# Kernel optimization log

Measured on AMD Instinct MI355X. Metric: run time of the kernel, lower is better.

## Reference

```python
import jax, jax.numpy as jnp
import numpy as np

EPS = 1e-12  # F.normalize eps

def _l2norm(v):
    n = jnp.sqrt(jnp.sum(v * v, axis=-1, keepdims=True))
    return v / jnp.maximum(n, EPS)

def setup_inputs() -> dict:
    key = jax.random.key(0)
    k1, k2, k3 = jax.random.split(key, 3)
    B, C, H, Wd = 32, 256, 64, 64
    M = 64
    x = jax.random.normal(k1, (B, C, H, Wd), dtype=jnp.float32)
    stdv = 1.0 / np.sqrt(M)
    W = jax.random.uniform(k2, (M, C), dtype=jnp.float32, minval=-stdv, maxval=stdv)
    label_batch = jax.random.randint(k3, (B,), 0, 2)
    return {"x": x, "W": W, "label_batch": label_batch}

def reference(x, W, label_batch):
    B, C, H, Wd = x.shape
    M = W.shape[0]
    # [B, HW, C] tokens; key == query == flattened input (pos=False)
    tok = x.transpose(0, 2, 3, 1).reshape(B, H * Wd, C)
    # per-pixel contribution to each prototype, softmax over pixels (dim=1)
    proto_weight = jax.nn.softmax(jnp.einsum('bnc,mc->bnm', tok, W), axis=1)
    # prototypes [B, M, C], L2-normalized
    proto = _l2norm(jnp.einsum('bnm,bnc->bmc', proto_weight, tok))
    # relevance of each pixel to each prototype, softmax over prototypes
    score = jax.nn.softmax(jnp.einsum('bnc,bmc->bnm', tok, proto), axis=-1)
    # reconstructed query
    new_query = _l2norm(jnp.einsum('bnm,bmc->bnc', score, proto))
    # compact loss: MSE(keys, nearest prototype) (new_cpt == 'True')
    top1 = jnp.argmax(score, axis=-1)                      # [B, HW]
    pos = jnp.take_along_axis(proto, top1[:, :, None], axis=1)  # [B, HW, C]
    compact_loss = jnp.mean((tok - pos) ** 2)
    # distance loss: push prototypes apart
    p2 = jnp.sum(proto * proto, axis=-1)                   # [B, M]
    sqd = p2[:, :, None] + p2[:, None, :] - 2.0 * jnp.einsum('bmc,bkc->bmk', proto, proto)
    dis = 1.0 - sqd
    dis = dis * (dis > 0).astype(dis.dtype)
    dis = jnp.triu(dis, k=1)
    dis_loss = jnp.mean(jnp.sum(dis, axis=(1, 2)) * 2.0 / (M * (M - 1)))
    out = new_query.transpose(0, 2, 1).reshape(B, C, H, Wd)
    return (out, compact_loss, dis_loss)
```

## Files before the change

### kernel.cpp

```cpp
#include <hip/hip_runtime.h>
#include <math.h>

#define B 32
#define C 256
#define M 64
#define N 4096

typedef __attribute__((ext_vector_type(8))) short s16x8;
typedef __attribute__((ext_vector_type(8))) __bf16 bf16x8;
typedef __attribute__((ext_vector_type(4))) float f32x4;
typedef __attribute__((ext_vector_type(4))) unsigned short u16x4;
typedef __attribute__((ext_vector_type(8))) unsigned short u16x8;

static constexpr float EPS = 1e-12f;

__device__ __forceinline__ unsigned short f2bf(float f) {
    unsigned u = __float_as_uint(f);
    u += 0x7FFFu + ((u >> 16) & 1u);
    return (unsigned short)(u >> 16);
}
__device__ __forceinline__ float bf2f(unsigned short h) {
    return __uint_as_float((unsigned)h << 16);
}
__device__ __forceinline__ f32x4 MFMA(s16x8 a, s16x8 b, f32x4 c) {
    return __builtin_amdgcn_mfma_f32_16x16x32_bf16(
        __builtin_bit_cast(bf16x8, a), __builtin_bit_cast(bf16x8, b), c, 0, 0, 0);
}
__device__ __forceinline__ s16x8 cvt8(const f32x4 a, const f32x4 b) {
    bf16x8 h;
    h[0] = (__bf16)a[0]; h[1] = (__bf16)a[1]; h[2] = (__bf16)a[2]; h[3] = (__bf16)a[3];
    h[4] = (__bf16)b[0]; h[5] = (__bf16)b[1]; h[6] = (__bf16)b[2]; h[7] = (__bf16)b[3];
    return __builtin_bit_cast(s16x8, h);
}
__device__ __forceinline__ int swz(int n) {
    return (((n >> 2) & 3) | ((n & 1) << 2)) << 3;
}

__global__ __launch_bounds__(256) void kW_convert(const float* __restrict__ Wf,
                                                  unsigned short* __restrict__ Wb) {
    const int i = blockIdx.x * 256 + threadIdx.x;
    Wb[i] = f2bf(Wf[i]);
}

__global__ __launch_bounds__(256) void k01(const float* __restrict__ x,
                                           const unsigned short* __restrict__ Wb,
                                           unsigned short* __restrict__ xbt,
                                           unsigned short* __restrict__ Sb,
                                           float* __restrict__ xsq) {
    const int nb = blockIdx.x, b = blockIdx.y;
    const int t = threadIdx.x;
    __shared__ unsigned short tsT[64 * 256];
    __shared__ float xred[16][68];
    const int nq = t & 15, cq = t >> 4;
    float part[4] = {0.f, 0.f, 0.f, 0.f};
    const float* xrow = x + (size_t)b * C * N + (size_t)nb * 64 + 4 * nq;
#pragma unroll
    for (int step = 0; step < 4; ++step) {
        const int c0 = cq * 4 + step * 64;
        f32x4 q[4];
#pragma unroll
        for (int i = 0; i < 4; ++i) q[i] = *(const f32x4*)(xrow + (size_t)(c0 + i) * N);
#pragma unroll
        for (int k = 0; k < 4; ++k) {
            const int n = 4 * nq + k;
            u16x4 h;
#pragma unroll
            for (int i = 0; i < 4; ++i) {
                part[k] += q[i][k] * q[i][k];
                h[i] = f2bf(q[i][k]);
            }
            *(u16x4*)(&tsT[n * 256 + (c0 ^ swz(n))]) = h;
        }
    }
#pragma unroll
    for (int k = 0; k < 4; ++k) xred[cq][4 * nq + k] = part[k];
    __syncthreads();
    if (t < 64) {
        float s = 0.f;
#pragma unroll
        for (int j = 0; j < 16; ++j) s += xred[j][t];
        xsq[(size_t)b * N + nb * 64 + t] = s;
    }
    {
        const int l = t & 31, nh = t >> 5;
#pragma unroll
        for (int j = 0; j < 8; ++j) {
            const int n = nh + 8 * j;
            const int c0 = l * 8;
            const u16x8 v = *(const u16x8*)(&tsT[n * 256 + (c0 ^ swz(n))]);
            *(u16x8*)(xbt + ((size_t)b * N + nb * 64 + n) * C + c0) = v;
        }
    }
    const int wv = t >> 6, lane = t & 63, li = lane & 15, lk = lane >> 4;
    const f32x4 zv = {0.f, 0.f, 0.f, 0.f};
    f32x4 acc[4] = {zv, zv, zv, zv};
    const unsigned short* br = Wb + (size_t)(wv * 16 + li) * C + lk * 8;
#pragma unroll
    for (int c0 = 0; c0 < C; c0 += 32) {
        const s16x8 bfrag = *(const s16x8*)(br + c0);
#pragma unroll
        for (int s = 0; s < 4; ++s) {
            const int n = s * 16 + li;
            const s16x8 a = *(const s16x8*)(&tsT[n * 256 + ((lk * 8 + c0) ^ swz(n))]);
            acc[s] = MFMA(a, bfrag, acc[s]);
        }
    }
    unsigned short* Srow = Sb + ((size_t)b * M + wv * 16 + li) * N + nb * 64;
#pragma unroll
    for (int s = 0; s < 4; ++s) {
        u16x4 h;
#pragma unroll
        for (int r = 0; r < 4; ++r) h[r] = f2bf(acc[s][r]);
        *(u16x4*)(Srow + s * 16 + lk * 4) = h;
    }
}

__global__ __launch_bounds__(256) void k2_softmax_n(const unsigned short* __restrict__ Sb,
                                                    unsigned short* __restrict__ Pb) {
    const int m = blockIdx.x, b = blockIdx.y;
    const unsigned short* col = Sb + ((size_t)b * M + m) * N;
    unsigned short* po = Pb + ((size_t)b * M + m) * N;
    const int t = threadIdx.x;
    float v[16];
    const u16x8 h0 = *(const u16x8*)(col + t * 16);
    const u16x8 h1 = *(const u16x8*)(col + t * 16 + 8);
#pragma unroll
    for (int i = 0; i < 8; ++i) v[i] = bf2f(h0[i]);
#pragma unroll
    for (int i = 0; i < 8; ++i) v[8 + i] = bf2f(h1[i]);
    float mx = -INFINITY;
#pragma unroll
    for (int i = 0; i < 16; ++i) mx = fmaxf(mx, v[i]);
#pragma unroll
    for (int off = 32; off >= 1; off >>= 1) mx = fmaxf(mx, __shfl_xor(mx, off));
    __shared__ float redm[4], reds[4];
    const int wave = t >> 6, lane = t & 63;
    if (lane == 0) redm[wave] = mx;
    __syncthreads();
    mx = fmaxf(fmaxf(redm[0], redm[1]), fmaxf(redm[2], redm[3]));
    float s = 0.f;
#pragma unroll
    for (int i = 0; i < 16; ++i) {
        v[i] = __expf(v[i] - mx);
        s += v[i];
    }
#pragma unroll
    for (int off = 32; off >= 1; off >>= 1) s += __shfl_xor(s, off);
    if (lane == 0) reds[wave] = s;
    __syncthreads();
    s = reds[0] + reds[1] + reds[2] + reds[3];
    const float inv = 1.f / s;
    u16x8 o0, o1;
#pragma unroll
    for (int i = 0; i < 8; ++i) o0[i] = f2bf(v[i] * inv);
#pragma unroll
    for (int i = 0; i < 8; ++i) o1[i] = f2bf(v[8 + i] * inv);
    *(u16x8*)(po + t * 16) = o0;
    *(u16x8*)(po + t * 16 + 8) = o1;
}

__global__ __launch_bounds__(256) void k3_mfma(const float* __restrict__ x,
                                               const unsigned short* __restrict__ Pb,
                                               float* __restrict__ parts) {
    const int ck = blockIdx.x, b = blockIdx.y;
    const int wv = threadIdx.x >> 6, lane = threadIdx.x & 63;
    const int li = lane & 15, lk = lane >> 4;
    const int c0w = wv * 64;
    const int nb = ck * 512;
    const f32x4 zv = {0.f, 0.f, 0.f, 0.f};
    f32x4 acc[4][4];
#pragma unroll
    for (int s = 0; s < 4; ++s)
#pragma unroll
        for (int u = 0; u < 4; ++u) acc[s][u] = zv;
    const float* ar = x + ((size_t)b * C + c0w + li) * N + nb + lk * 8;
    const unsigned short* br = Pb + ((size_t)b * M + li) * N + nb + lk * 8;
#pragma unroll 4
    for (int n0 = 0; n0 < 512; n0 += 32) {
        s16x8 af[4], bf_[4];
#pragma unroll
        for (int s = 0; s < 4; ++s) {
            const float* p = ar + (size_t)(s * 16) * N + n0;
            af[s] = cvt8(*(const f32x4*)p, *(const f32x4*)(p + 4));
        }
#pragma unroll
        for (int u = 0; u < 4; ++u) bf_[u] = *(const s16x8*)(br + (size_t)(u * 16) * N + n0);
#pragma unroll
        for (int s = 0; s < 4; ++s)
#pragma unroll
            for (int u = 0; u < 4; ++u) acc[s][u] = MFMA(af[s], bf_[u], acc[s][u]);
    }
    float* pp = parts + ((size_t)b * 8 + ck) * M * C;
#pragma unroll
    for (int s = 0; s < 4; ++s)
#pragma unroll
        for (int u = 0; u < 4; ++u)
            *(f32x4*)(pp + (size_t)(u * 16 + li) * C + c0w + s * 16 + lk * 4) = acc[s][u];
}

__global__ __launch_bounds__(256) void k3b_reduce(const float* __restrict__ parts,
                                                  unsigned short* __restrict__ proto_bf,
                                                  unsigned short* __restrict__ protoT_bf,
                                                  float* __restrict__ p2) {
    const int mb = blockIdx.x, b = blockIdx.y;
    const int t = threadIdx.x;
    const int ml = t >> 5, cl = t & 31;
    const int m = mb * 8 + ml;
    const int c0 = cl * 8;
    float v[8] = {0.f, 0.f, 0.f, 0.f, 0.f, 0.f, 0.f, 0.f};
    const float* pbase = parts + (size_t)b * 8 * M * C + (size_t)m * C + c0;
#pragma unroll
    for (int ck = 0; ck < 8; ++ck) {
        const f32x4 q0 = *(const f32x4*)(pbase + (size_t)ck * M * C);
        const f32x4 q1 = *(const f32x4*)(pbase + (size_t)ck * M * C + 4);
#pragma unroll
        for (int j = 0; j < 4; ++j) { v[j] += q0[j]; v[4 + j] += q1[j]; }
    }
    float sq = 0.f;
#pragma unroll
    for (int j = 0; j < 8; ++j) sq += v[j] * v[j];
#pragma unroll
    for (int off = 16; off >= 1; off >>= 1) sq += __shfl_xor(sq, off);
    const float denom = fmaxf(sqrtf(sq), EPS);
    const float scale = 1.f / denom;
    if (cl == 0) p2[b * M + m] = sq / (denom * denom);
    u16x8 h;
#pragma unroll
    for (int j = 0; j < 8; ++j) h[j] = f2bf(v[j] * scale);
    *(u16x8*)(proto_bf + ((size_t)b * M + m) * C + c0) = h;
#pragma unroll
    for (int j = 0; j < 8; ++j)
        protoT_bf[((size_t)b * C + c0 + j) * M + m] = h[j];
}

__global__ __launch_bounds__(512) void k4f(const unsigned short* __restrict__ proto_bf,
                                           const unsigned short* __restrict__ protoT_bf,
                                           const unsigned short* __restrict__ xbt,
                                           const float* __restrict__ p2,
                                           const float* __restrict__ xsq,
                                           float* __restrict__ out,
                                           float* __restrict__ cparts) {
    const int b = blockIdx.y;
    const int t = threadIdx.x;
    const int w = t >> 6, lane = t & 63, li = lane & 15, lk = lane >> 4;
    const int nblk = blockIdx.x * 256;
    __shared__ unsigned short p_lds[256 * 64];
    __shared__ float red2[2][256];
    __shared__ float red8[8];
    const f32x4 zv = {0.f, 0.f, 0.f, 0.f};
    f32x4 acc[4][2];
#pragma unroll
    for (int s = 0; s < 4; ++s)
#pragma unroll
        for (int u = 0; u < 2; ++u) acc[s][u] = zv;
    const unsigned short* ar = proto_bf + (size_t)b * M * C + (size_t)li * C + lk * 8;
    const unsigned short* br = xbt + ((size_t)b * N + nblk + w * 32 + li) * C + lk * 8;
#pragma unroll
    for (int c0 = 0; c0 < C; c0 += 32) {
        s16x8 af[4], bf_[2];
#pragma unroll
        for (int s = 0; s < 4; ++s) af[s] = *(const s16x8*)(ar + (size_t)(s * 16) * C + c0);
#pragma unroll
        for (int u = 0; u < 2; ++u) bf_[u] = *(const s16x8*)(br + (size_t)(u * 16) * C + c0);
#pragma unroll
        for (int s = 0; s < 4; ++s)
#pragma unroll
            for (int u = 0; u < 2; ++u) acc[s][u] = MFMA(af[s], bf_[u], acc[s][u]);
    }
    float csum = 0.f;
#pragma unroll
    for (int u = 0; u < 2; ++u) {
        const int n = nblk + w * 32 + u * 16 + li;
        const int nl = w * 32 + u * 16 + li;
        float vmax = -INFINITY;
#pragma unroll
        for (int s = 0; s < 4; ++s)
#pragma unroll
            for (int r = 0; r < 4; ++r) vmax = fmaxf(vmax, acc[s][u][r]);
        vmax = fmaxf(vmax, __shfl_xor(vmax, 16));
        vmax = fmaxf(vmax, __shfl_xor(vmax, 32));
        int t1 = 1 << 30;
#pragma unroll
        for (int s = 0; s < 4; ++s)
#pragma unroll
            for (int r = 0; r < 4; ++r)
                if (acc[s][u][r] == vmax) t1 = min(t1, s * 16 + lk * 4 + r);
        t1 = min(t1, __shfl_xor(t1, 16));
        t1 = min(t1, __shfl_xor(t1, 32));
        float es = 0.f;
#pragma unroll
        for (int s = 0; s < 4; ++s)
#pragma unroll
            for (int r = 0; r < 4; ++r) {
                const float e = __expf(acc[s][u][r] - vmax);
                acc[s][u][r] = e;
                es += e;
            }
        es += __shfl_xor(es, 16);
        es += __shfl_xor(es, 32);
        const float inv = 1.f / es;
#pragma unroll
        for (int s = 0; s < 4; ++s) {
            u16x4 h;
#pragma unroll
            for (int r = 0; r < 4; ++r) h[r] = f2bf(acc[s][u][r] * inv);
            const unsigned off =
                (unsigned)((nl * 128 + ((s * 16 + lk * 4) << 1)) ^ ((nl & 7) << 4));
            *(u16x4*)((char*)p_lds + off) = h;
        }
        if (lk == 0) csum += xsq[(size_t)b * N + n] - 2.f * vmax + p2[b * M + t1];
    }
#pragma unroll
    for (int off = 32; off >= 1; off >>= 1) csum += __shfl_xor(csum, off);
    if (lane == 0) red8[w] = csum;
    __syncthreads();
    if (t == 0) {
        float cs = 0.f;
#pragma unroll
        for (int j = 0; j < 8; ++j) cs += red8[j];
        cparts[b * 16 + blockIdx.x] = cs;
    }
    const int nq = w & 3, ch = w >> 2;
    f32x4 a2[4][8];
#pragma unroll
    for (int s = 0; s < 4; ++s)
#pragma unroll
        for (int u = 0; u < 8; ++u) a2[s][u] = zv;
    const unsigned short* br2 =
        protoT_bf + ((size_t)b * C + ch * 128 + li) * M + lk * 8;
#pragma unroll
    for (int m0 = 0; m0 < M; m0 += 32) {
        s16x8 af2[4], bf2[8];
#pragma unroll
        for (int s = 0; s < 4; ++s) {
            const int nl = nq * 64 + s * 16 + li;
            const unsigned off =
                (unsigned)((nl * 128 + ((m0 + lk * 8) << 1)) ^ ((nl & 7) << 4));
            af2[s] = *(const s16x8*)((const char*)p_lds + off);
        }
#pragma unroll
        for (int u = 0; u < 8; ++u)
            bf2[u] = *(const s16x8*)(br2 + (size_t)(u * 16) * M + m0);
#pragma unroll
        for (int s = 0; s < 4; ++s)
#pragma unroll
            for (int u = 0; u < 8; ++u) a2[s][u] = MFMA(af2[s], bf2[u], a2[s][u]);
    }
    float ssq[4][4];
#pragma unroll
    for (int s = 0; s < 4; ++s)
#pragma unroll
        for (int r = 0; r < 4; ++r) {
            float sum = 0.f;
#pragma unroll
            for (int u = 0; u < 8; ++u) sum += a2[s][u][r] * a2[s][u][r];
#pragma unroll
            for (int off = 8; off >= 1; off >>= 1) sum += __shfl_xor(sum, off);
            ssq[s][r] = sum;
        }
    if (li == 0) {
#pragma unroll
        for (int s = 0; s < 4; ++s)
#pragma unroll
            for (int r = 0; r < 4; ++r)
                red2[ch][nq * 64 + s * 16 + lk * 4 + r] = ssq[s][r];
    }
    __syncthreads();
    float scl[4][4];
#pragma unroll
    for (int s = 0; s < 4; ++s)
#pragma unroll
        for (int r = 0; r < 4; ++r) {
            const int nl = nq * 64 + s * 16 + lk * 4 + r;
            scl[s][r] = 1.f / fmaxf(sqrtf(red2[0][nl] + red2[1][nl]), EPS);
        }
    float* ob = out + (size_t)b * C * N;
#pragma unroll
    for (int s = 0; s < 4; ++s)
#pragma unroll
        for (int u = 0; u < 8; ++u) {
            const int c = ch * 128 + u * 16 + li;
            f32x4 q;
#pragma unroll
            for (int r = 0; r < 4; ++r) q[r] = a2[s][u][r] * scl[s][r];
            *(f32x4*)(ob + (size_t)c * N + nblk + nq * 64 + s * 16 + lk * 4) = q;
        }
}

__global__ __launch_bounds__(256) void k4_score(const unsigned short* __restrict__ proto_bf,
                                                const unsigned short* __restrict__ xbt,
                                                const float* __restrict__ p2,
                                                const float* __restrict__ xsq,
                                                unsigned short* __restrict__ pnm,
                                                float* __restrict__ cparts) {
    const int b = blockIdx.y;
    const int wv = threadIdx.x >> 6, lane = threadIdx.x & 63;
    const int li = lane & 15, lk = lane >> 4;
    const int nbase = blockIdx.x * 256 + wv * 64;
    const f32x4 zv = {0.f, 0.f, 0.f, 0.f};
    f32x4 acc[4][4];
#pragma unroll
    for (int s = 0; s < 4; ++s)
#pragma unroll
        for (int u = 0; u < 4; ++u) acc[s][u] = zv;
    const unsigned short* ar = proto_bf + ((size_t)b * M + li) * C + lk * 8;
    const unsigned short* br = xbt + ((size_t)b * N + nbase + li) * C + lk * 8;
#pragma unroll
    for (int c0 = 0; c0 < C; c0 += 32) {
        s16x8 af[4], bf_[4];
#pragma unroll
        for (int s = 0; s < 4; ++s) af[s] = *(const s16x8*)(ar + (size_t)(s * 16) * C + c0);
#pragma unroll
        for (int u = 0; u < 4; ++u) bf_[u] = *(const s16x8*)(br + (size_t)(u * 16) * C + c0);
#pragma unroll
        for (int s = 0; s < 4; ++s)
#pragma unroll
            for (int u = 0; u < 4; ++u) acc[s][u] = MFMA(af[s], bf_[u], acc[s][u]);
    }
    float csum = 0.f;
#pragma unroll
    for (int u = 0; u < 4; ++u) {
        const int n = nbase + u * 16 + li;
        float vmax = -INFINITY;
#pragma unroll
        for (int s = 0; s < 4; ++s)
#pragma unroll
            for (int r = 0; r < 4; ++r) vmax = fmaxf(vmax, acc[s][u][r]);
        vmax = fmaxf(vmax, __shfl_xor(vmax, 16));
        vmax = fmaxf(vmax, __shfl_xor(vmax, 32));
        int t1 = 1 << 30;
#pragma unroll
        for (int s = 0; s < 4; ++s)
#pragma unroll
            for (int r = 0; r < 4; ++r)
                if (acc[s][u][r] == vmax) t1 = min(t1, s * 16 + lk * 4 + r);
        t1 = min(t1, __shfl_xor(t1, 16));
        t1 = min(t1, __shfl_xor(t1, 32));
        float es = 0.f;
#pragma unroll
        for (int s = 0; s < 4; ++s)
#pragma unroll
            for (int r = 0; r < 4; ++r) {
                const float e = __expf(acc[s][u][r] - vmax);
                acc[s][u][r] = e;
                es += e;
            }
        es += __shfl_xor(es, 16);
        es += __shfl_xor(es, 32);
        const float inv = 1.f / es;
        unsigned short* prow = pnm + ((size_t)b * N + n) * M;
#pragma unroll
        for (int s = 0; s < 4; ++s) {
            u16x4 h;
#pragma unroll
            for (int r = 0; r < 4; ++r) h[r] = f2bf(acc[s][u][r] * inv);
            *(u16x4*)(prow + s * 16 + lk * 4) = h;
        }
        if (lk == 0) csum += xsq[(size_t)b * N + n] - 2.f * vmax + p2[b * M + t1];
    }
#pragma unroll
    for (int off = 32; off >= 1; off >>= 1) csum += __shfl_xor(csum, off);
    __shared__ float red[4];
    if (lane == 0) red[wv] = csum;
    __syncthreads();
    if (threadIdx.x == 0)
        cparts[b * 16 + blockIdx.x] = red[0] + red[1] + red[2] + red[3];
}

__global__ __launch_bounds__(256) void k4b_mfma(const unsigned short* __restrict__ pnm,
                                                const unsigned short* __restrict__ protoT_bf,
                                                float* __restrict__ out) {
    const int b = blockIdx.y;
    const int wv = threadIdx.x >> 6, lane = threadIdx.x & 63;
    const int li = lane & 15, lk = lane >> 4;
    const int n0 = blockIdx.x * 64;
    const int cb = wv * 64;
    const f32x4 zv = {0.f, 0.f, 0.f, 0.f};
    f32x4 acc[4][4];
#pragma unroll
    for (int s = 0; s < 4; ++s)
#pragma unroll
        for (int u = 0; u < 4; ++u) acc[s][u] = zv;
    const unsigned short* ar = pnm + ((size_t)b * N + n0 + li) * M + lk * 8;
    const unsigned short* br = protoT_bf + ((size_t)b * C + cb + li) * M + lk * 8;
#pragma unroll
    for (int m0 = 0; m0 < M; m0 += 32) {
        s16x8 af[4], bf_[4];
#pragma unroll
        for (int s = 0; s < 4; ++s) af[s] = *(const s16x8*)(ar + (size_t)(s * 16) * M + m0);
#pragma unroll
        for (int u = 0; u < 4; ++u) bf_[u] = *(const s16x8*)(br + (size_t)(u * 16) * M + m0);
#pragma unroll
        for (int s = 0; s < 4; ++s)
#pragma unroll
            for (int u = 0; u < 4; ++u) acc[s][u] = MFMA(af[s], bf_[u], acc[s][u]);
    }
    __shared__ float ls[4][64];
    __shared__ float ls2[64];
    float psq[4][4];
#pragma unroll
    for (int s = 0; s < 4; ++s)
#pragma unroll
        for (int r = 0; r < 4; ++r) {
            float sum = 0.f;
#pragma unroll
            for (int u = 0; u < 4; ++u) sum += acc[s][u][r] * acc[s][u][r];
#pragma unroll
            for (int off = 8; off >= 1; off >>= 1) sum += __shfl_xor(sum, off);
            psq[s][r] = sum;
        }
    if (li == 0) {
#pragma unroll
        for (int s = 0; s < 4; ++s)
#pragma unroll
            for (int r = 0; r < 4; ++r) ls[wv][s * 16 + lk * 4 + r] = psq[s][r];
    }
    __syncthreads();
    if (threadIdx.x < 64) {
        const int tt = threadIdx.x;
        const float tot = ls[0][tt] + ls[1][tt] + ls[2][tt] + ls[3][tt];
        ls2[tt] = 1.f / fmaxf(sqrtf(tot), EPS);
    }
    __syncthreads();
    float scl[4][4];
#pragma unroll
    for (int s = 0; s < 4; ++s)
#pragma unroll
        for (int r = 0; r < 4; ++r) scl[s][r] = ls2[s * 16 + lk * 4 + r];
    float* ob = out + (size_t)b * C * N;
#pragma unroll
    for (int s = 0; s < 4; ++s)
#pragma unroll
        for (int u = 0; u < 4; ++u) {
            f32x4 q;
#pragma unroll
            for (int r = 0; r < 4; ++r) q[r] = acc[s][u][r] * scl[s][r];
            *(f32x4*)(ob + (size_t)(cb + u * 16 + li) * N + n0 + s * 16 + lk * 4) = q;
        }
}

__global__ __launch_bounds__(256) void k5_dis(const unsigned short* __restrict__ proto_bf,
                                              const float* __restrict__ p2,
                                              float* __restrict__ dparts) {
    const int q = blockIdx.x;
    const int b = blockIdx.y;
    const unsigned short* pr = proto_bf + (size_t)b * M * C;
    __shared__ float pl[M * C];
    for (int idx = threadIdx.x; idx < M * C; idx += 256) {
        int m = idx >> 8, c = idx & 255;
        pl[m * 256 + (c ^ (m & 31))] = bf2f(pr[idx]);
    }
    __syncthreads();
    float sum = 0.f;
    for (int k = 0; k < 2; ++k) {
        const int pair = q * 512 + k * 256 + threadIdx.x;
        const int i = pair >> 6, j = pair & 63;
        if (j > i) {
            float g = 0.f;
#pragma unroll 8
            for (int c = 0; c < C; ++c)
                g += pl[i * 256 + (c ^ (i & 31))] * pl[j * 256 + (c ^ (j & 31))];
            const float d = 1.f - (p2[b * M + i] + p2[b * M + j] - 2.f * g);
            sum += fmaxf(d, 0.f);
        }
    }
#pragma unroll
    for (int off = 32; off >= 1; off >>= 1) sum += __shfl_xor(sum, off);
    __shared__ float red[4];
    const int wave = threadIdx.x >> 6, lane = threadIdx.x & 63;
    if (lane == 0) red[wave] = sum;
    __syncthreads();
    if (threadIdx.x == 0) dparts[b * 8 + q] = red[0] + red[1] + red[2] + red[3];
}

__global__ __launch_bounds__(256) void k6_final(const float* __restrict__ cparts,
                                                const float* __restrict__ dparts,
                                                float* __restrict__ losses) {
    const int t = threadIdx.x;
    float cs = cparts[t] + cparts[t + 256];
    float ds = dparts[t];
#pragma unroll
    for (int off = 32; off >= 1; off >>= 1) {
        cs += __shfl_xor(cs, off);
        ds += __shfl_xor(ds, off);
    }
    __shared__ float rc[4], rd[4];
    const int wave = t >> 6, lane = t & 63;
    if (lane == 0) { rc[wave] = cs; rd[wave] = ds; }
    __syncthreads();
    if (t == 0) {
        const float ctot = rc[0] + rc[1] + rc[2] + rc[3];
        const float dtot = rd[0] + rd[1] + rd[2] + rd[3];
        losses[0] = ctot / ((float)B * (float)N * (float)C);
        losses[1] = dtot * (2.f / (float)(M * (M - 1))) / (float)B;
    }
}

extern "C" void kernel_launch(void* const* d_in, const int* in_sizes, int n_in,
                              void* d_out, int out_size, void* d_ws, size_t ws_size,
                              hipStream_t stream) {
    const float* x = (const float*)d_in[0];
    const float* Wf = (const float*)d_in[1];
    float* out = (float*)d_out;
    float* wsf = (float*)d_ws;
    float* losses = out + (size_t)B * C * N;

    const bool big = ws_size >= (size_t)69774336;

    if (big) {
        unsigned short* Sbf = (unsigned short*)out;
        float* parts = out + 4194304;
        unsigned short* Pbf = (unsigned short*)(out + 8388608);
        unsigned short* xbt = (unsigned short*)wsf;
        float* xsq = wsf + 16777216;
        unsigned short* proto_bf = (unsigned short*)(wsf + 16908288);
        unsigned short* protoT_bf = (unsigned short*)(wsf + 17170432);
        unsigned short* Wb = (unsigned short*)(wsf + 17432576);
        float* p2 = wsf + 17440768;
        float* cparts = wsf + 17442816;
        float* dparts = wsf + 17443328;

        kW_convert<<<dim3(64), 256, 0, stream>>>(Wf, Wb);
        k01<<<dim3(N / 64, B), 256, 0, stream>>>(x, Wb, xbt, Sbf, xsq);
        k2_softmax_n<<<dim3(M, B), 256, 0, stream>>>(Sbf, Pbf);
        k3_mfma<<<dim3(8, B), 256, 0, stream>>>(x, Pbf, parts);
        k3b_reduce<<<dim3(8, B), 256, 0, stream>>>(parts, proto_bf, protoT_bf, p2);
        k4f<<<dim3(N / 256, B), 512, 0, stream>>>(proto_bf, protoT_bf, xbt, p2, xsq,
                                                  out, cparts);
        k5_dis<<<dim3(8, B), 256, 0, stream>>>(proto_bf, p2, dparts);
        k6_final<<<1, 256, 0, stream>>>(cparts, dparts, losses);
    } else {
        unsigned short* xbt = (unsigned short*)d_out;
        unsigned short* Sbf = (unsigned short*)wsf;
        float* parts = wsf;
        unsigned short* Pbf = (unsigned short*)(wsf + 4194304);
        unsigned short* pnm = Pbf;
        float* xsq = wsf + 8388608;
        unsigned short* proto_bf = (unsigned short*)(wsf + 8519680);
        unsigned short* protoT_bf = (unsigned short*)(wsf + 8781824);
        unsigned short* Wb = (unsigned short*)(wsf + 9043968);
        float* p2 = wsf + 9052160;
        float* cparts = wsf + 9054208;
        float* dparts = wsf + 9054720;

        kW_convert<<<dim3(64), 256, 0, stream>>>(Wf, Wb);
        k01<<<dim3(N / 64, B), 256, 0, stream>>>(x, Wb, xbt, Sbf, xsq);
        k2_softmax_n<<<dim3(M, B), 256, 0, stream>>>(Sbf, Pbf);
        k3_mfma<<<dim3(8, B), 256, 0, stream>>>(x, Pbf, parts);
        k3b_reduce<<<dim3(8, B), 256, 0, stream>>>(parts, proto_bf, protoT_bf, p2);
        k4_score<<<dim3(N / 256, B), 256, 0, stream>>>(proto_bf, xbt, p2, xsq, pnm, cparts);
        k4b_mfma<<<dim3(N / 64, B), 256, 0, stream>>>(pnm, protoT_bf, out);
        k5_dis<<<dim3(8, B), 256, 0, stream>>>(proto_bf, p2, dparts);
        k6_final<<<1, 256, 0, stream>>>(cparts, dparts, losses);
    }
}
```

Measured before the change: 194.7 us.

## Fold W conversion into k01, shrink fused score block, drop softmax normalization

Removes the separate W-to-bf16 kernel by converting W on the fly inside k01. It also skips the per-pixel softmax sum and divide, because the result is L2-normalized afterwards and the scale cancels. The fused score/reconstruct kernel now uses 256-thread blocks over 128 pixels with two blocks per CU, halving LDS per block for better occupancy. The final loss reduction takes a variable part count. Unnormalized exps stored in bf16 keep precision similar, since max-subtracted values stay at most 1.

Result: no change. 192.9 us (-0.9%).

```diff
diff --git a/kernel.cpp b/kernel.cpp
--- a/kernel.cpp
+++ b/kernel.cpp
@@ -36,14 +36,8 @@
     return (((n >> 2) & 3) | ((n & 1) << 2)) << 3;
 }
 
-__global__ __launch_bounds__(256) void kW_convert(const float* __restrict__ Wf,
-                                                  unsigned short* __restrict__ Wb) {
-    const int i = blockIdx.x * 256 + threadIdx.x;
-    Wb[i] = f2bf(Wf[i]);
-}
-
 __global__ __launch_bounds__(256) void k01(const float* __restrict__ x,
-                                           const unsigned short* __restrict__ Wb,
+                                           const float* __restrict__ Wf,
                                            unsigned short* __restrict__ xbt,
                                            unsigned short* __restrict__ Sb,
                                            float* __restrict__ xsq) {
@@ -94,10 +88,10 @@
     const int wv = t >> 6, lane = t & 63, li = lane & 15, lk = lane >> 4;
     const f32x4 zv = {0.f, 0.f, 0.f, 0.f};
     f32x4 acc[4] = {zv, zv, zv, zv};
-    const unsigned short* br = Wb + (size_t)(wv * 16 + li) * C + lk * 8;
+    const float* wr = Wf + (size_t)(wv * 16 + li) * C + lk * 8;
 #pragma unroll
     for (int c0 = 0; c0 < C; c0 += 32) {
-        const s16x8 bfrag = *(const s16x8*)(br + c0);
+        const s16x8 bfrag = cvt8(*(const f32x4*)(wr + c0), *(const f32x4*)(wr + c0 + 4));
 #pragma unroll
         for (int s = 0; s < 4; ++s) {
             const int n = s * 16 + li;
@@ -233,20 +227,20 @@
         protoT_bf[((size_t)b * C + c0 + j) * M + m] = h[j];
 }
 
-__global__ __launch_bounds__(512) void k4f(const unsigned short* __restrict__ proto_bf,
-                                           const unsigned short* __restrict__ protoT_bf,
-                                           const unsigned short* __restrict__ xbt,
-                                           const float* __restrict__ p2,
-                                           const float* __restrict__ xsq,
-                                           float* __restrict__ out,
-                                           float* __restrict__ cparts) {
+__global__ __launch_bounds__(256, 2) void k4f2(const unsigned short* __restrict__ proto_bf,
+                                               const unsigned short* __restrict__ protoT_bf,
+                                               const unsigned short* __restrict__ xbt,
+                                               const float* __restrict__ p2,
+                                               const float* __restrict__ xsq,
+                                               float* __restrict__ out,
+                                               float* __restrict__ cparts) {
     const int b = blockIdx.y;
     const int t = threadIdx.x;
     const int w = t >> 6, lane = t & 63, li = lane & 15, lk = lane >> 4;
-    const int nblk = blockIdx.x * 256;
-    __shared__ unsigned short p_lds[256 * 64];
-    __shared__ float red2[2][256];
-    __shared__ float red8[8];
+    const int nblk = blockIdx.x * 128;
+    __shared__ unsigned short p_lds[128 * 64];
+    __shared__ float red2[2][128];
+    __shared__ float red4[4];
     const f32x4 zv = {0.f, 0.f, 0.f, 0.f};
     f32x4 acc[4][2];
 #pragma unroll
@@ -287,23 +281,11 @@
                 if (acc[s][u][r] == vmax) t1 = min(t1, s * 16 + lk * 4 + r);
         t1 = min(t1, __shfl_xor(t1, 16));
         t1 = min(t1, __shfl_xor(t1, 32));
-        float es = 0.f;
-#pragma unroll
-        for (int s = 0; s < 4; ++s)
-#pragma unroll
-            for (int r = 0; r < 4; ++r) {
-                const float e = __expf(acc[s][u][r] - vmax);
-                acc[s][u][r] = e;
-                es += e;
-            }
-        es += __shfl_xor(es, 16);
-        es += __shfl_xor(es, 32);
-        const float inv = 1.f / es;
 #pragma unroll
         for (int s = 0; s < 4; ++s) {
             u16x4 h;
 #pragma unroll
-            for (int r = 0; r < 4; ++r) h[r] = f2bf(acc[s][u][r] * inv);
+            for (int r = 0; r < 4; ++r) h[r] = f2bf(__expf(acc[s][u][r] - vmax));
             const unsigned off =
                 (unsigned)((nl * 128 + ((s * 16 + lk * 4) << 1)) ^ ((nl & 7) << 4));
             *(u16x4*)((char*)p_lds + off) = h;
@@ -312,22 +294,16 @@
     }
 #pragma unroll
     for (int off = 32; off >= 1; off >>= 1) csum += __shfl_xor(csum, off);
-    if (lane == 0) red8[w] = csum;
-    __syncthreads();
-    if (t == 0) {
-        float cs = 0.f;
-#pragma unroll
-        for (int j = 0; j < 8; ++j) cs += red8[j];
-        cparts[b * 16 + blockIdx.x] = cs;
-    }
-    const int nq = w & 3, ch = w >> 2;
+    if (lane == 0) red4[w] = csum;
+    __syncthreads();
+    if (t == 0) cparts[b * 32 + blockIdx.x] = red4[0] + red4[1] + red4[2] + red4[3];
+    const int nq = w & 1, ch = w >> 1;
     f32x4 a2[4][8];
 #pragma unroll
     for (int s = 0; s < 4; ++s)
 #pragma unroll
         for (int u = 0; u < 8; ++u) a2[s][u] = zv;
-    const unsigned short* br2 =
-        protoT_bf + ((size_t)b * C + ch * 128 + li) * M + lk * 8;
+    const unsigned short* br2 = protoT_bf + ((size_t)b * C + ch * 128 + li) * M + lk * 8;
 #pragma unroll
     for (int m0 = 0; m0 < M; m0 += 32) {
         s16x8 af2[4], bf2[8];
@@ -436,24 +412,12 @@
                 if (acc[s][u][r] == vmax) t1 = min(t1, s * 16 + lk * 4 + r);
         t1 = min(t1, __shfl_xor(t1, 16));
         t1 = min(t1, __shfl_xor(t1, 32));
-        float es = 0.f;
-#pragma unroll
-        for (int s = 0; s < 4; ++s)
-#pragma unroll
-            for (int r = 0; r < 4; ++r) {
-                const float e = __expf(acc[s][u][r] - vmax);
-                acc[s][u][r] = e;
-                es += e;
-            }
-        es += __shfl_xor(es, 16);
-        es += __shfl_xor(es, 32);
-        const float inv = 1.f / es;
         unsigned short* prow = pnm + ((size_t)b * N + n) * M;
 #pragma unroll
         for (int s = 0; s < 4; ++s) {
             u16x4 h;
 #pragma unroll
-            for (int r = 0; r < 4; ++r) h[r] = f2bf(acc[s][u][r] * inv);
+            for (int r = 0; r < 4; ++r) h[r] = f2bf(__expf(acc[s][u][r] - vmax));
             *(u16x4*)(prow + s * 16 + lk * 4) = h;
         }
         if (lk == 0) csum += xsq[(size_t)b * N + n] - 2.f * vmax + p2[b * M + t1];
@@ -573,11 +537,12 @@
     if (threadIdx.x == 0) dparts[b * 8 + q] = red[0] + red[1] + red[2] + red[3];
 }
 
-__global__ __launch_bounds__(256) void k6_final(const float* __restrict__ cparts,
+__global__ __launch_bounds__(256) void k6_final(const float* __restrict__ cparts, int ncp,
                                                 const float* __restrict__ dparts,
                                                 float* __restrict__ losses) {
     const int t = threadIdx.x;
-    float cs = cparts[t] + cparts[t + 256];
+    float cs = 0.f;
+    for (int i = t; i < ncp; i += 256) cs += cparts[i];
     float ds = dparts[t];
 #pragma unroll
     for (int off = 32; off >= 1; off >>= 1) {
@@ -605,7 +570,7 @@
     float* wsf = (float*)d_ws;
     float* losses = out + (size_t)B * C * N;
 
-    const bool big = ws_size >= (size_t)69774336;
+    const bool big = ws_size >= (size_t)69743616;
 
     if (big) {
         unsigned short* Sbf = (unsigned short*)out;
@@ -615,20 +580,18 @@
         float* xsq = wsf + 16777216;
         unsigned short* proto_bf = (unsigned short*)(wsf + 16908288);
         unsigned short* protoT_bf = (unsigned short*)(wsf + 17170432);
-        unsigned short* Wb = (unsigned short*)(wsf + 17432576);
-        float* p2 = wsf + 17440768;
-        float* cparts = wsf + 17442816;
-        float* dparts = wsf + 17443328;
-
-        kW_convert<<<dim3(64), 256, 0, stream>>>(Wf, Wb);
-        k01<<<dim3(N / 64, B), 256, 0, stream>>>(x, Wb, xbt, Sbf, xsq);
+        float* p2 = wsf + 17432576;
+        float* cparts = wsf + 17434624;
+        float* dparts = wsf + 17435648;
+
+        k01<<<dim3(N / 64, B), 256, 0, stream>>>(x, Wf, xbt, Sbf, xsq);
         k2_softmax_n<<<dim3(M, B), 256, 0, stream>>>(Sbf, Pbf);
         k3_mfma<<<dim3(8, B), 256, 0, stream>>>(x, Pbf, parts);
         k3b_reduce<<<dim3(8, B), 256, 0, stream>>>(parts, proto_bf, protoT_bf, p2);
-        k4f<<<dim3(N / 256, B), 512, 0, stream>>>(proto_bf, protoT_bf, xbt, p2, xsq,
-                                                  out, cparts);
+        k4f2<<<dim3(N / 128, B), 256, 0, stream>>>(proto_bf, protoT_bf, xbt, p2, xsq,
+                                                   out, cparts);
         k5_dis<<<dim3(8, B), 256, 0, stream>>>(proto_bf, p2, dparts);
-        k6_final<<<1, 256, 0, stream>>>(cparts, dparts, losses);
+        k6_final<<<1, 256, 0, stream>>>(cparts, B * 32, dparts, losses);
     } else {
         unsigned short* xbt = (unsigned short*)d_out;
         unsigned short* Sbf = (unsigned short*)wsf;
@@ -638,19 +601,17 @@
         float* xsq = wsf + 8388608;
         unsigned short* proto_bf = (unsigned short*)(wsf + 8519680);
         unsigned short* protoT_bf = (unsigned short*)(wsf + 8781824);
-        unsigned short* Wb = (unsigned short*)(wsf + 9043968);
         float* p2 = wsf + 9052160;
         float* cparts = wsf + 9054208;
         float* dparts = wsf + 9054720;
 
-        kW_convert<<<dim3(64), 256, 0, stream>>>(Wf, Wb);
-        k01<<<dim3(N / 64, B), 256, 0, stream>>>(x, Wb, xbt, Sbf, xsq);
+        k01<<<dim3(N / 64, B), 256, 0, stream>>>(x, Wf, xbt, Sbf, xsq);
         k2_softmax_n<<<dim3(M, B), 256, 0, stream>>>(Sbf, Pbf);
         k3_mfma<<<dim3(8, B), 256, 0, stream>>>(x, Pbf, parts);
         k3b_reduce<<<dim3(8, B), 256, 0, stream>>>(parts, proto_bf, protoT_bf, p2);
         k4_score<<<dim3(N / 256, B), 256, 0, stream>>>(proto_bf, xbt, p2, xsq, pnm, cparts);
         k4b_mfma<<<dim3(N / 64, B), 256, 0, stream>>>(pnm, protoT_bf, out);
         k5_dis<<<dim3(8, B), 256, 0, stream>>>(proto_bf, p2, dparts);
-        k6_final<<<1, 256, 0, stream>>>(cparts, dparts, losses);
-    }
-}
+        k6_final<<<1, 256, 0, stream>>>(cparts, B * 16, dparts, losses);
+    }
+}
```
